# Optimization experiments

Hardware: AMD Instinct MI355X
Metric: run time of the kernel (lower is better)

The kernel has to match this reference:

```python
import jax, jax.numpy as jnp
import numpy as np

B, T, D = 2, 2048, 2048
H, HD, RD = 16, 192, 64
CD = HD - RD          # 128 content dims per head
QR, DL = 768, 512     # q lora rank, kv latent dim
THETA = 10000.0


def setup_inputs() -> dict:
    key = jax.random.key(0)
    ks = jax.random.split(key, 9)
    s = 0.02
    return {
        "x": jax.random.normal(ks[0], (B, T, D), jnp.float32),
        "wq_down": jax.random.normal(ks[1], (D, QR), jnp.float32) * s,
        "wq_up": jax.random.normal(ks[2], (QR, H * CD), jnp.float32) * s,
        "wq_rope": jax.random.normal(ks[3], (D, H * RD), jnp.float32) * s,
        "wkv_down": jax.random.normal(ks[4], (D, DL), jnp.float32) * s,
        "wk_up": jax.random.normal(ks[5], (DL, H * CD), jnp.float32) * s,
        "wv_up": jax.random.normal(ks[6], (DL, H * HD), jnp.float32) * s,
        "wk_rope": jax.random.normal(ks[7], (D, H * RD), jnp.float32) * s,
        "wo": jax.random.normal(ks[8], (H * HD, D), jnp.float32) * s,
    }


def _rope_tables(seq_len):
    inv = 1.0 / (THETA ** (jnp.arange(0, RD, 2, dtype=jnp.float32) / RD))  # [RD/2]
    ang = jnp.arange(seq_len, dtype=jnp.float32)[:, None] * inv[None, :]  # [T, RD/2]
    return jnp.cos(ang), jnp.sin(ang)


def _apply_rope(x, cos, sin):
    # x: [B,H,T,RD]; cos/sin: [T,RD/2] broadcast over B,H
    d = RD // 2
    x1, x2 = x[..., :d], x[..., d:]
    return jnp.concatenate([x1 * cos - x2 * sin, x1 * sin + x2 * cos], axis=-1)


def reference(x, wq_down, wq_up, wq_rope, wkv_down, wk_up, wv_up, wk_rope, wo):
    # projections
    q_c = (x @ wq_down) @ wq_up                       # [B,T,H*CD]
    q_p = x @ wq_rope                                 # [B,T,H*RD]
    latent = x @ wkv_down                             # [B,T,DL]
    k_c = latent @ wk_up                              # [B,T,H*CD]
    k_p = x @ wk_rope                                 # [B,T,H*RD]
    v = latent @ wv_up                                # [B,T,H*HD]

    def heads(t, d):
        return t.reshape(B, T, H, d).transpose(0, 2, 1, 3)  # [B,H,T,d]

    q_c, q_p = heads(q_c, CD), heads(q_p, RD)
    k_c, k_p = heads(k_c, CD), heads(k_p, RD)
    v = heads(v, HD)

    cos, sin = _rope_tables(T)
    q_p = _apply_rope(q_p, cos, sin)
    k_p = _apply_rope(k_p, cos, sin)

    q = jnp.concatenate([q_c, q_p], axis=-1)          # [B,H,T,HD]
    k = jnp.concatenate([k_c, k_p], axis=-1)          # [B,H,T,HD]

    scale = 1.0 / jnp.sqrt(jnp.asarray(HD, q.dtype))
    scores = jnp.einsum("bhqd,bhkd->bhqk", q, k) * scale
    causal = jnp.tril(jnp.ones((T, T), dtype=bool))
    scores = jnp.where(causal, scores, jnp.finfo(scores.dtype).min)
    attn = jax.nn.softmax(scores, axis=-1)
    out = jnp.einsum("bhqk,bhkd->bhqd", attn, v)      # [B,H,T,HD]
    out = out.transpose(0, 2, 1, 3).reshape(B, T, H * HD)
    return out @ wo                                   # [B,T,D]
```

## Files before the change

### kernel.cpp

```cpp
#include <hip/hip_runtime.h>
#include <hip/hip_bf16.h>
#include <cstdint>
#include <cstddef>

typedef __bf16 bf16_t;
typedef __bf16 bf16x8 __attribute__((ext_vector_type(8)));
typedef float f32x4 __attribute__((ext_vector_type(4)));

#define MFMA16(a, b, c) __builtin_amdgcn_mfma_f32_16x16x32_bf16((a), (b), (c), 0, 0, 0)

__device__ __forceinline__ void gload_lds16(const void* g, void* l) {
  __builtin_amdgcn_global_load_lds((__attribute__((address_space(1))) void*)(g),
                                   (__attribute__((address_space(3))) void*)(l),
                                   16, 0, 0);
}

__device__ __forceinline__ uint32_t pkbf(float lo, float hi) {
  union { bf16_t h[2]; uint32_t u; } u2;
  u2.h[0] = (bf16_t)lo; u2.h[1] = (bf16_t)hi;
  return u2.u;
}

__global__ __launch_bounds__(256) void cvt_f32_to_bf16(const float* __restrict__ in,
                                                       bf16_t* __restrict__ out) {
  size_t i = ((size_t)blockIdx.x * 256 + threadIdx.x) * 4;
  float4 v = *(const float4*)(in + i);
  bf16_t o[4] = {(bf16_t)v.x, (bf16_t)v.y, (bf16_t)v.z, (bf16_t)v.w};
  *(uint2*)(out + i) = *(uint2*)o;
}

__global__ __launch_bounds__(256) void transpose_w(const float* __restrict__ in,
                                                   bf16_t* __restrict__ out, int R, int C) {
  __shared__ bf16_t tile[32][33];
  int c0 = blockIdx.x * 32, r0 = blockIdx.y * 32;
  int tx = threadIdx.x, ty = threadIdx.y;
#pragma unroll
  for (int s = 0; s < 4; s++) {
    int r = ty + s * 8;
    tile[r][tx] = (bf16_t)in[(size_t)(r0 + r) * C + c0 + tx];
  }
  __syncthreads();
#pragma unroll
  for (int s = 0; s < 4; s++) {
    int r = ty + s * 8;
    out[(size_t)(c0 + r) * R + r0 + tx] = tile[tx][r];
  }
}

__global__ __launch_bounds__(256) void transpose_v_kernel(const bf16_t* __restrict__ v,
                                                          bf16_t* __restrict__ vt) {
  __shared__ bf16_t tile[32][33];
  int bh = blockIdx.z;
  int t0 = blockIdx.x * 32, d0 = blockIdx.y * 32;
  int tx = threadIdx.x, ty = threadIdx.y;
  const bf16_t* src = v + (size_t)(bh >> 4) * 2048 * 3072 + (bh & 15) * 192;
#pragma unroll
  for (int s = 0; s < 4; s++) {
    int t = ty + s * 8;
    tile[t][tx] = src[(size_t)(t0 + t) * 3072 + d0 + tx];
  }
  __syncthreads();
  bf16_t* dst = vt + (size_t)bh * 192 * 2048;
#pragma unroll
  for (int s = 0; s < 4; s++) {
    int d = ty + s * 8;
    dst[(size_t)(d0 + d) * 2048 + t0 + tx] = tile[tx][d];
  }
}

__global__ __launch_bounds__(256) void rope_inplace(bf16_t* __restrict__ buf) {
  int idx = blockIdx.x * 256 + threadIdx.x;
  int j = idx & 31;
  int h = (idx >> 5) & 15;
  int row = idx >> 9;
  int t = row & 2047;
  size_t base = (size_t)row * 3072 + h * 192 + 128;
  float inv = expf(-(float)j * 0.28782313662425574f);
  float ang = (float)t * inv;
  float c, s;
  sincosf(ang, &s, &c);
  float x1 = (float)buf[base + j];
  float x2 = (float)buf[base + j + 32];
  buf[base + j]      = (bf16_t)(x1 * c - x2 * s);
  buf[base + j + 32] = (bf16_t)(x1 * s + x2 * c);
}

template <int MODE>
__global__ __launch_bounds__(256) void gemm_bt(const bf16_t* __restrict__ A, int lda,
                                               const bf16_t* __restrict__ Bt,
                                               void* __restrict__ C0, void* __restrict__ C1,
                                               void* __restrict__ C2, int K, int ldc) {
  __shared__ __align__(16) bf16_t sA[128 * 64];
  __shared__ __align__(16) bf16_t sB[128 * 64];
  const int tid = threadIdx.x;
  const int l = tid & 63, w = tid >> 6;
  const int l15 = l & 15, l4 = l >> 4;
  const int wr = w >> 1, wc = w & 1;
  const int m0 = blockIdx.y * 128, n0 = blockIdx.x * 128;

  f32x4 acc[4][4] = {};

  for (int kt = 0; kt < K; kt += 64) {
#pragma unroll
    for (int r = 0; r < 4; r++) {
      int i = r * 256 + tid;
      int row = i >> 3, cl = i & 7;
      int cg = cl ^ (row & 7);
      const bf16_t* srcA = A + (size_t)(m0 + row) * lda + kt + cg * 8;
      const bf16_t* srcB = Bt + (size_t)(n0 + row) * K + kt + cg * 8;
      char* dstA = (char*)sA + (size_t)(r * 256 + w * 64) * 16;
      char* dstB = (char*)sB + (size_t)(r * 256 + w * 64) * 16;
      gload_lds16(srcA, dstA);
      gload_lds16(srcB, dstB);
    }
    __syncthreads();
#pragma unroll
    for (int ks = 0; ks < 2; ks++) {
      bf16x8 af[4], bfr[4];
#pragma unroll
      for (int mf = 0; mf < 4; mf++) {
        int row = wr * 64 + mf * 16 + l15;
        int cl = (ks * 4 + l4) ^ (row & 7);
        af[mf] = *(const bf16x8*)(sA + row * 64 + cl * 8);
      }
#pragma unroll
      for (int nf = 0; nf < 4; nf++) {
        int row = wc * 64 + nf * 16 + l15;
        int cl = (ks * 4 + l4) ^ (row & 7);
        bfr[nf] = *(const bf16x8*)(sB + row * 64 + cl * 8);
      }
#pragma unroll
      for (int mf = 0; mf < 4; mf++)
#pragma unroll
        for (int nf = 0; nf < 4; nf++)
          acc[mf][nf] = MFMA16(af[mf], bfr[nf], acc[mf][nf]);
    }
    __syncthreads();
  }

#pragma unroll
  for (int mf = 0; mf < 4; mf++)
#pragma unroll
    for (int nf = 0; nf < 4; nf++)
#pragma unroll
      for (int r = 0; r < 4; r++) {
        int m = m0 + wr * 64 + mf * 16 + l4 * 4 + r;
        int n = n0 + wc * 64 + nf * 16 + l15;
        float v = acc[mf][nf][r];
        if constexpr (MODE == 1) {
          ((float*)C0)[(size_t)m * ldc + n] = v;
        } else if constexpr (MODE == 2) {
          ((bf16_t*)C0)[(size_t)m * 3072 + (n >> 7) * 192 + (n & 127)] = (bf16_t)v;
        } else if constexpr (MODE == 4) {
          if (n < 1280) {
            ((bf16_t*)C0)[(size_t)m * 1280 + n] = (bf16_t)v;
          } else if (n < 2304) {
            int nn = n - 1280;
            ((bf16_t*)C1)[(size_t)m * 3072 + (nn >> 6) * 192 + 128 + (nn & 63)] = (bf16_t)v;
          } else {
            int nn = n - 2304;
            ((bf16_t*)C2)[(size_t)m * 3072 + (nn >> 6) * 192 + 128 + (nn & 63)] = (bf16_t)v;
          }
        } else {
          if (n < 2048) {
            ((bf16_t*)C0)[(size_t)m * 3072 + (n >> 7) * 192 + (n & 127)] = (bf16_t)v;
          } else {
            ((bf16_t*)C1)[(size_t)m * 3072 + (n - 2048)] = (bf16_t)v;
          }
        }
      }
}

__global__ __launch_bounds__(512, 2) void attn_kernel(const bf16_t* __restrict__ q,
                                                      const bf16_t* __restrict__ kbuf,
                                                      const bf16_t* __restrict__ vt,
                                                      bf16_t* __restrict__ ao) {
  __shared__ __align__(16) bf16_t sK0[64][192];
  __shared__ __align__(16) bf16_t sK1[64][192];
  __shared__ __align__(16) bf16_t sV0[192][64];
  __shared__ __align__(16) bf16_t sV1[192][64];

  const int tid = threadIdx.x, l = tid & 63, w = tid >> 6;
  const int l15 = l & 15, l4 = (l >> 4) & 3;
  const int bh = blockIdx.x & 31;
  const int c = blockIdx.x >> 5;
  const int b = bh >> 4, h = bh & 15;
  const int ca = c, cb = 15 - c;
  const int ra = ca * 128 + w * 16;
  const int rb = cb * 128 + w * 16;
  const int tga = 2 * ca + (w >> 2);
  const int tgb = 2 * cb + (w >> 2);

  const bf16_t* qp = q + (size_t)b * 2048 * 3072 + h * 192;
  const bf16_t* kp = kbuf + (size_t)b * 2048 * 3072 + h * 192;
  const bf16_t* vp = vt + (size_t)bh * 192 * 2048;

  bf16x8 qf[2][6];
#pragma unroll
  for (int kd = 0; kd < 6; kd++) {
    qf[0][kd] = *(const bf16x8*)(qp + (size_t)(ra + l15) * 3072 + kd * 32 + l4 * 8);
    qf[1][kd] = *(const bf16x8*)(qp + (size_t)(rb + l15) * 3072 + kd * 32 + l4 * 8);
  }

  f32x4 o[2][12] = {};
  float mrow[2] = {-__builtin_inff(), -__builtin_inff()};
  float lrow[2] = {0.0f, 0.0f};

  const float scale = 0.07216878364870322f;
  const float THR = 7.0f;
  const int nkt = 2 * cb + 2;
  const int src0 = l15 + ((l4 & 1) << 5);
  const int src1 = src0 + 16;
  const bool hibank = (l4 & 2) != 0;

#define STAGE(SK, SV, KT)                                                           \
  {                                                                                 \
    const int k0s = (KT) * 64;                                                      \
    _Pragma("unroll")                                                               \
    for (int r = 0; r < 3; r++) {                                                   \
      int i = r * 512 + tid;                                                        \
      int row = i / 24, cc = i % 24;                                                \
      int g = cc - (row & 7) * 3;                                                   \
      if (g < 0) g += 24;                                                           \
      gload_lds16(kp + (size_t)(k0s + row) * 3072 + g * 8,                          \
                  (char*)&SK[0][0] + (size_t)(r * 512 + w * 64) * 16);              \
    }                                                                               \
    _Pragma("unroll")                                                               \
    for (int r = 0; r < 3; r++) {                                                   \
      int i = r * 512 + tid;                                                        \
      int d = i >> 3, cc = i & 7;                                                   \
      gload_lds16(vp + (size_t)d * 2048 + k0s + (cc ^ (d & 7)) * 8,                 \
                  (char*)&SV[0][0] + (size_t)(r * 512 + w * 64) * 16);              \
    }                                                                               \
  }

#define SOFTMAX_CHUNK(c, rbase, tg)                                                    \
    {                                                                                  \
      const bool diag = (kt == (tg));                                                  \
      _Pragma("unroll")                                                                \
      for (int nf = 0; nf < 4; nf++)                                                   \
        _Pragma("unroll")                                                              \
        for (int r = 0; r < 4; r++) {                                                  \
          float sv = s[c][nf][r] * scale;                                              \
          if (diag) {                                                                  \
            int ktok = k0 + nf * 16 + l4 * 4 + r;                                      \
            if (ktok > (rbase) + l15) sv = -__builtin_inff();                          \
          }                                                                            \
          s[c][nf][r] = sv;                                                            \
        }                                                                              \
      float m_in = s[c][0][0];                                                         \
      _Pragma("unroll")                                                                \
      for (int nf = 0; nf < 4; nf++)                                                   \
        _Pragma("unroll")                                                              \
        for (int r = 0; r < 4; r++)                                                    \
          if (nf | r) m_in = fmaxf(m_in, s[c][nf][r]);                                 \
      m_in = fmaxf(m_in, __shfl_xor(m_in, 16));                                        \
      m_in = fmaxf(m_in, __shfl_xor(m_in, 32));                                        \
      if (!__all(m_in - mrow[c] <= THR)) {                                             \
        float mn = fmaxf(mrow[c], m_in);                                               \
        float alpha = __expf(mrow[c] - mn);                                            \
        mrow[c] = mn;                                                                  \
        lrow[c] *= alpha;                                                              \
        f32x4 av;                                                                      \
        _Pragma("unroll")                                                              \
        for (int r = 0; r < 4; r++) av[r] = __shfl(alpha, l4 * 4 + r);                 \
        _Pragma("unroll")                                                              \
        for (int nf2 = 0; nf2 < 12; nf2++) o[c][nf2] *= av;                            \
      }                                                                                \
      float rs = 0.0f;                                                                 \
      _Pragma("unroll")                                                                \
      for (int nf = 0; nf < 4; nf++)                                                   \
        _Pragma("unroll")                                                              \
        for (int r = 0; r < 4; r++) {                                                  \
          float pv = __expf(s[c][nf][r] - mrow[c]);                                    \
          s[c][nf][r] = pv;                                                            \
          rs += pv;                                                                    \
        }                                                                              \
      rs += __shfl_xor(rs, 16);                                                        \
      rs += __shfl_xor(rs, 32);                                                        \
      lrow[c] += rs;                                                                   \
      uint32_t wq[8];                                                                  \
      _Pragma("unroll")                                                                \
      for (int nf = 0; nf < 4; nf++) {                                                 \
        wq[nf * 2 + 0] = pkbf(s[c][nf][0], s[c][nf][1]);                               \
        wq[nf * 2 + 1] = pkbf(s[c][nf][2], s[c][nf][3]);                               \
      }                                                                                \
      _Pragma("unroll")                                                                \
      for (int ks = 0; ks < 2; ks++) {                                                 \
        uint32_t A0 = __shfl(wq[(2 * ks) * 2 + 0], src0);                              \
        uint32_t A1 = __shfl(wq[(2 * ks) * 2 + 1], src0);                              \
        uint32_t B0 = __shfl(wq[(2 * ks + 1) * 2 + 0], src0);                          \
        uint32_t B1 = __shfl(wq[(2 * ks + 1) * 2 + 1], src0);                          \
        uint32_t C0w = __shfl(wq[(2 * ks) * 2 + 0], src1);                             \
        uint32_t C1w = __shfl(wq[(2 * ks) * 2 + 1], src1);                             \
        uint32_t D0 = __shfl(wq[(2 * ks + 1) * 2 + 0], src1);                          \
        uint32_t D1 = __shfl(wq[(2 * ks + 1) * 2 + 1], src1);                          \
        union { uint32_t u[4]; bf16x8 v; } fr;                                         \
        fr.u[0] = hibank ? B0 : A0;                                                    \
        fr.u[1] = hibank ? B1 : A1;                                                    \
        fr.u[2] = hibank ? D0 : C0w;                                                   \
        fr.u[3] = hibank ? D1 : C1w;                                                   \
        pa[c][ks] = fr.v;                                                              \
      }                                                                                \
    }

#define TILE_BODY(SK, SV, KT)                                                          \
  {                                                                                    \
    const int kt = (KT);                                                               \
    const int k0 = kt * 64;                                                            \
    const bool act_a = (kt <= tga);                                                    \
    const bool act_b = (kt <= tgb);                                                    \
    f32x4 s[2][4] = {};                                                                \
    _Pragma("unroll")                                                                  \
    for (int kd = 0; kd < 6; kd++) {                                                   \
      bf16x8 bk[4];                                                                    \
      _Pragma("unroll")                                                                \
      for (int nf = 0; nf < 4; nf++) {                                                 \
        int row = nf * 16 + l15;                                                       \
        int cl = kd * 4 + l4 + (row & 7) * 3;                                          \
        if (cl >= 24) cl -= 24;                                                        \
        bk[nf] = *(const bf16x8*)(&SK[row][cl * 8]);                                   \
      }                                                                                \
      if (act_b) {                                                                     \
        _Pragma("unroll")                                                              \
        for (int nf = 0; nf < 4; nf++)                                                 \
          s[1][nf] = MFMA16(bk[nf], qf[1][kd], s[1][nf]);                              \
      }                                                                                \
      if (act_a) {                                                                     \
        _Pragma("unroll")                                                              \
        for (int nf = 0; nf < 4; nf++)                                                 \
          s[0][nf] = MFMA16(bk[nf], qf[0][kd], s[0][nf]);                              \
      }                                                                                \
    }                                                                                  \
    bf16x8 pa[2][2] = {};                                                              \
    if (act_b) SOFTMAX_CHUNK(1, rb, tgb)                                               \
    if (act_a) SOFTMAX_CHUNK(0, ra, tga)                                               \
    _Pragma("unroll")                                                                  \
    for (int ks = 0; ks < 2; ks++) {                                                   \
      _Pragma("unroll")                                                                \
      for (int nf2 = 0; nf2 < 12; nf2++) {                                             \
        int d = nf2 * 16 + l15;                                                        \
        int cl = (ks * 4 + l4) ^ (d & 7);                                              \
        bf16x8 vb = *(const bf16x8*)(&SV[d][cl * 8]);                                  \
        if (act_b) o[1][nf2] = MFMA16(pa[1][ks], vb, o[1][nf2]);                       \
        if (act_a) o[0][nf2] = MFMA16(pa[0][ks], vb, o[0][nf2]);                       \
      }                                                                                \
    }                                                                                  \
  }

  STAGE(sK0, sV0, 0)
  __syncthreads();

  for (int kt0 = 0; kt0 < nkt; kt0 += 2) {
    STAGE(sK1, sV1, kt0 + 1)
    TILE_BODY(sK0, sV0, kt0)
    __syncthreads();
    if (kt0 + 2 < nkt) STAGE(sK0, sV0, kt0 + 2)
    TILE_BODY(sK1, sV1, kt0 + 1)
    __syncthreads();
  }
#undef STAGE
#undef SOFTMAX_CHUNK
#undef TILE_BODY

#pragma unroll
  for (int mf = 0; mf < 2; mf++) {
    const int rbase = (mf == 0) ? ra : rb;
#pragma unroll
    for (int r = 0; r < 4; r++) {
      float lv = __shfl(lrow[mf], l4 * 4 + r);
      float inv = 1.0f / lv;
      int qrow = rbase + l4 * 4 + r;
#pragma unroll
      for (int nf2 = 0; nf2 < 12; nf2++) {
        int d = nf2 * 16 + l15;
        ao[(size_t)(b * 2048 + qrow) * 3072 + h * 192 + d] = (bf16_t)(o[mf][nf2][r] * inv);
      }
    }
  }
}

extern "C" void kernel_launch(void* const* d_in, const int* in_sizes, int n_in,
                              void* d_out, int out_size, void* d_ws, size_t ws_size,
                              hipStream_t stream) {
  const float* x       = (const float*)d_in[0];
  const float* wq_down = (const float*)d_in[1];
  const float* wq_up   = (const float*)d_in[2];
  const float* wq_rope = (const float*)d_in[3];
  const float* wkv_down= (const float*)d_in[4];
  const float* wk_up   = (const float*)d_in[5];
  const float* wv_up   = (const float*)d_in[6];
  const float* wk_rope = (const float*)d_in[7];
  const float* wo      = (const float*)d_in[8];
  float* out = (float*)d_out;

  char* p = (char*)d_ws;
  auto take = [&](size_t elems) { bf16_t* r = (bf16_t*)p; p += elems * 2; return r; };
  bf16_t* xb    = take(4096ull * 2048);
  bf16_t* fw1   = take(3328ull * 2048);
  bf16_t* wqu_t = take(2048ull * 768);
  bf16_t* fw2   = take(5120ull * 512);
  bf16_t* wo_t  = take(2048ull * 3072);
  bf16_t* qkvd  = take(4096ull * 1280);
  bf16_t* qbuf  = take(4096ull * 3072);
  bf16_t* kbuf  = take(4096ull * 3072);
  bf16_t* vbuf  = take(4096ull * 3072);
  bf16_t* vt    = take(4096ull * 3072);
  bf16_t* ao    = vbuf;

  dim3 tb(32, 8);
  cvt_f32_to_bf16<<<8192, 256, 0, stream>>>(x, xb);
  transpose_w<<<dim3(24, 64), tb, 0, stream>>>(wq_down,  fw1,                 2048, 768);
  transpose_w<<<dim3(16, 64), tb, 0, stream>>>(wkv_down, fw1 + 768ull * 2048, 2048, 512);
  transpose_w<<<dim3(32, 64), tb, 0, stream>>>(wq_rope,  fw1 + 1280ull * 2048,2048, 1024);
  transpose_w<<<dim3(32, 64), tb, 0, stream>>>(wk_rope,  fw1 + 2304ull * 2048,2048, 1024);
  transpose_w<<<dim3(64, 24), tb, 0, stream>>>(wq_up,    wqu_t,               768, 2048);
  transpose_w<<<dim3(64, 16), tb, 0, stream>>>(wk_up,    fw2,                 512, 2048);
  transpose_w<<<dim3(96, 16), tb, 0, stream>>>(wv_up,    fw2 + 2048ull * 512, 512, 3072);
  transpose_w<<<dim3(64, 96), tb, 0, stream>>>(wo,       wo_t,                3072, 2048);

  gemm_bt<4><<<dim3(26, 32), 256, 0, stream>>>(xb, 2048, fw1, qkvd, qbuf, kbuf, 2048, 0);
  gemm_bt<2><<<dim3(16, 32), 256, 0, stream>>>(qkvd, 1280, wqu_t, qbuf, nullptr, nullptr, 768, 0);
  gemm_bt<5><<<dim3(40, 32), 256, 0, stream>>>(qkvd + 768, 1280, fw2, kbuf, vbuf, nullptr, 512, 0);

  rope_inplace<<<8192, 256, 0, stream>>>(qbuf);
  rope_inplace<<<8192, 256, 0, stream>>>(kbuf);
  transpose_v_kernel<<<dim3(64, 6, 32), tb, 0, stream>>>(vbuf, vt);

  attn_kernel<<<256, 512, 0, stream>>>(qbuf, kbuf, vt, ao);

  gemm_bt<1><<<dim3(16, 32), 256, 0, stream>>>(ao, 3072, wo_t, out, nullptr, nullptr, 3072, 2048);
}
```

Baseline: 384.0 us.

## Double-buffer GEMM LDS tiles with 256x128 blocks of 512 threads

Replaces the single-buffered 128x128 GEMM with a 256x128 tile computed by 8 waves, using two LDS buffers. The next k-tile's global-to-LDS loads are issued before computing the current one, with explicit vmcnt waits and barriers. This is meant to overlap memory latency with MFMA work and raise per-block reuse of the B tile. LDS use grows to 96KB per block, and the grid halves, which may lower occupancy and leave CUs idle on the smaller GEMMs.

```diff
diff --git a/kernel.cpp b/kernel.cpp
--- a/kernel.cpp
+++ b/kernel.cpp
@@ -86,57 +86,86 @@
 }
 
 template <int MODE>
-__global__ __launch_bounds__(256) void gemm_bt(const bf16_t* __restrict__ A, int lda,
-                                               const bf16_t* __restrict__ Bt,
-                                               void* __restrict__ C0, void* __restrict__ C1,
-                                               void* __restrict__ C2, int K, int ldc) {
-  __shared__ __align__(16) bf16_t sA[128 * 64];
-  __shared__ __align__(16) bf16_t sB[128 * 64];
+__global__ __launch_bounds__(512, 2) void gemm_bt2(const bf16_t* __restrict__ A, int lda,
+                                                   const bf16_t* __restrict__ Bt,
+                                                   void* __restrict__ C0, void* __restrict__ C1,
+                                                   void* __restrict__ C2, int K, int ldc) {
+  __shared__ __align__(16) bf16_t sA0[256 * 64];
+  __shared__ __align__(16) bf16_t sB0[128 * 64];
+  __shared__ __align__(16) bf16_t sA1[256 * 64];
+  __shared__ __align__(16) bf16_t sB1[128 * 64];
   const int tid = threadIdx.x;
   const int l = tid & 63, w = tid >> 6;
-  const int l15 = l & 15, l4 = l >> 4;
+  const int l15 = l & 15, l4 = (l >> 4) & 3;
   const int wr = w >> 1, wc = w & 1;
-  const int m0 = blockIdx.y * 128, n0 = blockIdx.x * 128;
+  const int m0 = blockIdx.y * 256, n0 = blockIdx.x * 128;
+  const int nt = K >> 6;
 
   f32x4 acc[4][4] = {};
 
-  for (int kt = 0; kt < K; kt += 64) {
-#pragma unroll
-    for (int r = 0; r < 4; r++) {
-      int i = r * 256 + tid;
-      int row = i >> 3, cl = i & 7;
-      int cg = cl ^ (row & 7);
-      const bf16_t* srcA = A + (size_t)(m0 + row) * lda + kt + cg * 8;
-      const bf16_t* srcB = Bt + (size_t)(n0 + row) * K + kt + cg * 8;
-      char* dstA = (char*)sA + (size_t)(r * 256 + w * 64) * 16;
-      char* dstB = (char*)sB + (size_t)(r * 256 + w * 64) * 16;
-      gload_lds16(srcA, dstA);
-      gload_lds16(srcB, dstB);
+#define STAGEG(SA, SB, KT)                                                          \
+  {                                                                                 \
+    const int kts = (KT) * 64;                                                      \
+    _Pragma("unroll")                                                               \
+    for (int r = 0; r < 4; r++) {                                                   \
+      int i = r * 512 + tid;                                                        \
+      int row = i >> 3, cl = i & 7;                                                 \
+      int cg = cl ^ (row & 7);                                                      \
+      gload_lds16(A + (size_t)(m0 + row) * lda + kts + cg * 8,                      \
+                  (char*)(SA) + (size_t)(r * 512 + w * 64) * 16);                   \
+    }                                                                               \
+    _Pragma("unroll")                                                               \
+    for (int r = 0; r < 2; r++) {                                                   \
+      int i = r * 512 + tid;                                                        \
+      int row = i >> 3, cl = i & 7;                                                 \
+      int cg = cl ^ (row & 7);                                                      \
+      gload_lds16(Bt + (size_t)(n0 + row) * K + kts + cg * 8,                       \
+                  (char*)(SB) + (size_t)(r * 512 + w * 64) * 16);                   \
+    }                                                                               \
+  }
+
+#define GCOMPUTE(SA, SB)                                                            \
+  {                                                                                 \
+    _Pragma("unroll")                                                               \
+    for (int ks = 0; ks < 2; ks++) {                                                \
+      bf16x8 af[4], bfr[4];                                                         \
+      _Pragma("unroll")                                                             \
+      for (int mf = 0; mf < 4; mf++) {                                              \
+        int row = wr * 64 + mf * 16 + l15;                                          \
+        int cl = (ks * 4 + l4) ^ (row & 7);                                         \
+        af[mf] = *(const bf16x8*)((SA) + row * 64 + cl * 8);                        \
+      }                                                                             \
+      _Pragma("unroll")                                                             \
+      for (int nf = 0; nf < 4; nf++) {                                              \
+        int row = wc * 64 + nf * 16 + l15;                                          \
+        int cl = (ks * 4 + l4) ^ (row & 7);                                         \
+        bfr[nf] = *(const bf16x8*)((SB) + row * 64 + cl * 8);                       \
+      }                                                                             \
+      _Pragma("unroll")                                                             \
+      for (int mf = 0; mf < 4; mf++)                                                \
+        _Pragma("unroll")                                                           \
+        for (int nf = 0; nf < 4; nf++)                                              \
+          acc[mf][nf] = MFMA16(af[mf], bfr[nf], acc[mf][nf]);                       \
+    }                                                                               \
+  }
+
+  STAGEG(sA0, sB0, 0)
+  for (int t = 0; t < nt; t += 2) {
+    STAGEG(sA1, sB1, t + 1)
+    asm volatile("s_waitcnt vmcnt(6)\n\ts_barrier" ::: "memory");
+    GCOMPUTE(sA0, sB0)
+    asm volatile("s_barrier" ::: "memory");
+    if (t + 2 < nt) {
+      STAGEG(sA0, sB0, t + 2)
+      asm volatile("s_waitcnt vmcnt(6)\n\ts_barrier" ::: "memory");
+    } else {
+      asm volatile("s_waitcnt vmcnt(0)\n\ts_barrier" ::: "memory");
     }
-    __syncthreads();
-#pragma unroll
-    for (int ks = 0; ks < 2; ks++) {
-      bf16x8 af[4], bfr[4];
-#pragma unroll
-      for (int mf = 0; mf < 4; mf++) {
-        int row = wr * 64 + mf * 16 + l15;
-        int cl = (ks * 4 + l4) ^ (row & 7);
-        af[mf] = *(const bf16x8*)(sA + row * 64 + cl * 8);
-      }
-#pragma unroll
-      for (int nf = 0; nf < 4; nf++) {
-        int row = wc * 64 + nf * 16 + l15;
-        int cl = (ks * 4 + l4) ^ (row & 7);
-        bfr[nf] = *(const bf16x8*)(sB + row * 64 + cl * 8);
-      }
-#pragma unroll
-      for (int mf = 0; mf < 4; mf++)
-#pragma unroll
-        for (int nf = 0; nf < 4; nf++)
-          acc[mf][nf] = MFMA16(af[mf], bfr[nf], acc[mf][nf]);
-    }
-    __syncthreads();
-  }
+    GCOMPUTE(sA1, sB1)
+    asm volatile("s_barrier" ::: "memory");
+  }
+#undef STAGEG
+#undef GCOMPUTE
 
 #pragma unroll
   for (int mf = 0; mf < 4; mf++)
@@ -419,9 +448,9 @@
   transpose_w<<<dim3(96, 16), tb, 0, stream>>>(wv_up,    fw2 + 2048ull * 512, 512, 3072);
   transpose_w<<<dim3(64, 96), tb, 0, stream>>>(wo,       wo_t,                3072, 2048);
 
-  gemm_bt<4><<<dim3(26, 32), 256, 0, stream>>>(xb, 2048, fw1, qkvd, qbuf, kbuf, 2048, 0);
-  gemm_bt<2><<<dim3(16, 32), 256, 0, stream>>>(qkvd, 1280, wqu_t, qbuf, nullptr, nullptr, 768, 0);
-  gemm_bt<5><<<dim3(40, 32), 256, 0, stream>>>(qkvd + 768, 1280, fw2, kbuf, vbuf, nullptr, 512, 0);
+  gemm_bt2<4><<<dim3(26, 16), 512, 0, stream>>>(xb, 2048, fw1, qkvd, qbuf, kbuf, 2048, 0);
+  gemm_bt2<2><<<dim3(16, 16), 512, 0, stream>>>(qkvd, 1280, wqu_t, qbuf, nullptr, nullptr, 768, 0);
+  gemm_bt2<5><<<dim3(40, 16), 512, 0, stream>>>(qkvd + 768, 1280, fw2, kbuf, vbuf, nullptr, 512, 0);
 
   rope_inplace<<<8192, 256, 0, stream>>>(qbuf);
   rope_inplace<<<8192, 256, 0, stream>>>(kbuf);
@@ -429,5 +458,5 @@
 
   attn_kernel<<<256, 512, 0, stream>>>(qbuf, kbuf, vt, ao);
 
-  gemm_bt<1><<<dim3(16, 32), 256, 0, stream>>>(ao, 3072, wo_t, out, nullptr, nullptr, 3072, 2048);
-}
+  gemm_bt2<1><<<dim3(16, 16), 512, 0, stream>>>(ao, 3072, wo_t, out, nullptr, nullptr, 3072, 2048);
+}
```

Result: faster. 373.3 us (-2.8%).
